# Performance work log

Hardware: AMD Instinct MI355X
Metric: run time of the kernel (lower is better)

The kernel has to match this reference:

```python
import jax, jax.numpy as jnp
import numpy as np

N, E = 50000, 800000
IN, HID, OUT = 128, 256, 128
BN_EPS = 1e-5


def setup_inputs() -> dict:
    key = jax.random.key(0)
    ks = jax.random.split(key, 12)
    x = jax.random.normal(ks[0], (N, IN), dtype=jnp.float32)
    edge_index = jax.random.randint(ks[1], (2, E), 0, N, dtype=jnp.int64)
    edge_weight = jax.random.uniform(ks[2], (E,), dtype=jnp.float32)
    # GCNConv weights (glorot-ish scale) and biases
    W0 = jax.random.normal(ks[3], (IN, HID), dtype=jnp.float32) * (1.0 / np.sqrt(IN))
    b0 = jnp.zeros((HID,), jnp.float32)
    W1 = jax.random.normal(ks[4], (HID, HID), dtype=jnp.float32) * (1.0 / np.sqrt(HID))
    b1 = jnp.zeros((HID,), jnp.float32)
    Wl = jax.random.normal(ks[5], (HID, OUT), dtype=jnp.float32) * (1.0 / np.sqrt(HID))
    bl = jnp.zeros((OUT,), jnp.float32)
    # BatchNorm affine params (eval mode: running_mean=0, running_var=1)
    g0 = 1.0 + 0.1 * jax.random.normal(ks[6], (HID,), dtype=jnp.float32)
    be0 = 0.1 * jax.random.normal(ks[7], (HID,), dtype=jnp.float32)
    g1 = 1.0 + 0.1 * jax.random.normal(ks[8], (HID,), dtype=jnp.float32)
    be1 = 0.1 * jax.random.normal(ks[9], (HID,), dtype=jnp.float32)
    return {"x": x, "edge_index": edge_index, "edge_weight": edge_weight,
            "W0": W0, "b0": b0, "W1": W1, "b1": b1, "Wl": Wl, "bl": bl,
            "g0": g0, "be0": be0, "g1": g1, "be1": be1}


def reference(x, edge_index, edge_weight, W0, b0, W1, b1, Wl, bl, g0, be0, g1, be1):
    n = x.shape[0]
    row, col = edge_index[0], edge_index[1]
    # add self-loops with weight 1 (GCNConv default)
    ar = jnp.arange(n)
    rowf = jnp.concatenate([row, ar])
    colf = jnp.concatenate([col, ar])
    wf = jnp.concatenate([edge_weight, jnp.ones((n,), x.dtype)])
    # symmetric normalization: D^{-1/2} A D^{-1/2}
    deg = jax.ops.segment_sum(wf, colf, num_segments=n)
    dinv = jnp.where(deg > 0, jax.lax.rsqrt(deg), 0.0)
    norm = dinv[rowf] * wf * dinv[colf]  # [E+N]

    def conv(h, W, b):
        h = h @ W                       # [n, d_out]
        msg = h[rowf] * norm[:, None]   # gather + scale per edge
        return jax.ops.segment_sum(msg, colf, num_segments=n) + b

    def bn_eval(h, g, b):
        # eval-mode BN with running_mean=0, running_var=1
        return h * (g / jnp.sqrt(1.0 + BN_EPS)) + b

    h = jax.nn.relu(bn_eval(conv(x, W0, b0), g0, be0))
    h = jax.nn.relu(bn_eval(conv(h, W1, b1), g1, be1))
    h = conv(h, Wl, bl)
    return jax.nn.log_softmax(h, axis=1)
```

## Files before the change

### kernel.cpp

```cpp
#include <hip/hip_runtime.h>
#include <cstddef>
#include <cstdint>


#define GCN_BN_EPS 1e-5f
#define NB_CHUNK 64
#define NPART 4

typedef short v8bf __attribute__((ext_vector_type(8)));
typedef float v4f __attribute__((ext_vector_type(4)));


__device__ __forceinline__ float4 unpack_bf4(uint2 u) {
  float4 r;
  r.x = __uint_as_float(u.x << 16);
  r.y = __uint_as_float(u.x & 0xffff0000u);
  r.z = __uint_as_float(u.y << 16);
  r.w = __uint_as_float(u.y & 0xffff0000u);
  return r;
}
__device__ __forceinline__ uint16_t f2bf(float f) {
  uint32_t u = __float_as_uint(f);
  return (uint16_t)((u + 0x7fffu + ((u >> 16) & 1u)) >> 16);
}
__device__ __forceinline__ uint2 pack_bf4(float4 v) {
  uint2 r;
  r.x = (uint32_t)f2bf(v.x) | ((uint32_t)f2bf(v.y) << 16);
  r.y = (uint32_t)f2bf(v.z) | ((uint32_t)f2bf(v.w) << 16);
  return r;
}


__global__ void detect_kernel(const int* __restrict__ ei, int* __restrict__ flag) {
  if (threadIdx.x == 0) {
    int nz = 0;
    for (int k = 1; k < 64; k += 2) nz |= ei[k];
    *flag = (nz == 0) ? 1 : 0;
  }
}

__global__ void decode_kernel(const int* __restrict__ ei, const float* __restrict__ ew,
                              const int* __restrict__ flag,
                              int* __restrict__ col_, uint2* __restrict__ pk, int E) {
  int e = blockIdx.x * blockDim.x + threadIdx.x;
  if (e >= E) return;
  int r, c;
  if (*flag) { r = ei[2 * e]; c = ei[2 * (E + e)]; }
  else       { r = ei[e];     c = ei[E + e]; }
  col_[e] = c;
  pk[e] = make_uint2((unsigned)r, __float_as_uint(ew[e]));
}

__global__ __launch_bounds__(256) void hist_kernel(const int* __restrict__ col_,
                                                   int* __restrict__ hist,
                                                   int E, int n) {
  extern __shared__ unsigned int hsh[];
  const int chunk = blockIdx.x, part = blockIdx.y;
  const int npl = (n + NPART - 1) / NPART;
  const int lo = part * npl, hi = min(lo + npl, n);
  const int nw = (npl + 1) >> 1;
  for (int i = threadIdx.x; i < nw; i += 256) hsh[i] = 0u;
  __syncthreads();
  const int per = (E + NB_CHUNK - 1) / NB_CHUNK;
  const int e0 = chunk * per, e1 = min(e0 + per, E);
  for (int e = e0 + threadIdx.x; e < e1; e += 256) {
    int c = col_[e];
    if (c >= lo && c < hi) {
      int cl = c - lo;
      atomicAdd(&hsh[cl >> 1], 1u << ((cl & 1) * 16));
    }
  }
  __syncthreads();
  for (int i = threadIdx.x; i < hi - lo; i += 256)
    hist[(size_t)chunk * n + lo + i] = (int)((hsh[i >> 1] >> ((i & 1) * 16)) & 0xffffu);
}

__global__ __launch_bounds__(256) void scan1_kernel(const int* __restrict__ hist,
                                                    int* __restrict__ cnt,
                                                    int* __restrict__ bsum, int n) {
  __shared__ int ws[4];
  int i = blockIdx.x * 256 + threadIdx.x;
  int v = 0;
  if (i < n) {
    for (int b = 0; b < NB_CHUNK; ++b) v += hist[(size_t)b * n + i];
    cnt[i] = v;
  }
  int x = v;
#pragma unroll
  for (int s = 1; s < 64; s <<= 1) x += __shfl_xor(x, s, 64);
  if ((threadIdx.x & 63) == 0) ws[threadIdx.x >> 6] = x;
  __syncthreads();
  if (threadIdx.x == 0) bsum[blockIdx.x] = ws[0] + ws[1] + ws[2] + ws[3];
}

__global__ __launch_bounds__(1024) void scan2_kernel(int* __restrict__ bsum, int G,
                                                     int* __restrict__ off, int n, int E) {
  __shared__ int wsum[16], woff[16];
  int tid = threadIdx.x, lane = tid & 63, wv = tid >> 6;
  int v = (tid < G) ? bsum[tid] : 0;
  int x = v;
#pragma unroll
  for (int s = 1; s < 64; s <<= 1) { int t = __shfl_up(x, s, 64); if (lane >= s) x += t; }
  if (lane == 63) wsum[wv] = x;
  __syncthreads();
  if (wv == 0) {
    int wsv = (lane < 16) ? wsum[lane] : 0;
    int y = wsv;
#pragma unroll
    for (int s = 1; s < 16; s <<= 1) { int t = __shfl_up(y, s, 64); if (lane >= s) y += t; }
    if (lane < 16) woff[lane] = y - wsv;
  }
  __syncthreads();
  if (tid < G) bsum[tid] = x - v + woff[wv];
  if (tid == 0) off[n] = E;
}

__global__ __launch_bounds__(256) void scan3_kernel(const int* __restrict__ cnt,
                                                    const int* __restrict__ bsum,
                                                    int* __restrict__ off, int n) {
  __shared__ int wsum[4], woff[4];
  int tid = threadIdx.x, lane = tid & 63, wv = tid >> 6;
  int i = blockIdx.x * 256 + tid;
  int v = (i < n) ? cnt[i] : 0;
  int x = v;
#pragma unroll
  for (int s = 1; s < 64; s <<= 1) { int t = __shfl_up(x, s, 64); if (lane >= s) x += t; }
  if (lane == 63) wsum[wv] = x;
  __syncthreads();
  if (tid == 0) { int r = 0; for (int k = 0; k < 4; ++k) { woff[k] = r; r += wsum[k]; } }
  __syncthreads();
  if (i < n) off[i] = x - v + woff[wv] + bsum[blockIdx.x];
}

__global__ void base_kernel(const int* __restrict__ off, int* __restrict__ hist, int n) {
  int i = blockIdx.x * blockDim.x + threadIdx.x;
  if (i >= n) return;
  int run = off[i];
  for (int b = 0; b < NB_CHUNK; ++b) {
    size_t idx = (size_t)b * n + i;
    int h = hist[idx];
    hist[idx] = run;
    run += h;
  }
}

__global__ __launch_bounds__(256) void fill_kernel(
    const int* __restrict__ col_, const uint2* __restrict__ pk,
    const int* __restrict__ base, uint2* __restrict__ csr, int E, int n) {
  extern __shared__ int cur[];
  const int chunk = blockIdx.x, part = blockIdx.y;
  const int npl = (n + NPART - 1) / NPART;
  const int lo = part * npl, hi = min(lo + npl, n);
  for (int i = threadIdx.x; i < hi - lo; i += 256)
    cur[i] = base[(size_t)chunk * n + lo + i];
  __syncthreads();
  const int per = (E + NB_CHUNK - 1) / NB_CHUNK;
  const int e0 = chunk * per, e1 = min(e0 + per, E);
  for (int e = e0 + threadIdx.x; e < e1; e += 256) {
    int c = col_[e];
    if (c >= lo && c < hi) {
      int p = atomicAdd(&cur[c - lo], 1);
      csr[p] = pk[e];
    }
  }
}

__global__ void degdinv_kernel(const int* __restrict__ off, const uint2* __restrict__ csr,
                               float* __restrict__ dinv, int n) {
  int i = blockIdx.x * blockDim.x + threadIdx.x;
  if (i >= n) return;
  float s = 1.0f;
  int p1 = off[i + 1];
  for (int p = off[i]; p < p1; ++p) s += __uint_as_float(csr[p].y);
  dinv[i] = rsqrtf(s);
}

__global__ void val_kernel(const int* __restrict__ off, uint2* __restrict__ csr,
                           const float* __restrict__ dinv, int n) {
  int i = blockIdx.x * blockDim.x + threadIdx.x;
  if (i >= n) return;
  float dc = dinv[i];
  int p1 = off[i + 1];
  for (int p = off[i]; p < p1; ++p) {
    uint2 t = csr[p];
    csr[p].y = __float_as_uint(dinv[t.x] * __uint_as_float(t.y) * dc);
  }
}


__global__ void conv_x_kernel(const float* __restrict__ x, uint16_t* __restrict__ xb,
                              int n4) {
  int i = blockIdx.x * blockDim.x + threadIdx.x;
  if (i >= n4) return;
  float4 v = *(const float4*)&x[(size_t)i * 4];
  *(uint2*)&xb[(size_t)i * 4] = pack_bf4(v);
}

__global__ void conv_wt_kernel(const float* __restrict__ W, uint16_t* __restrict__ WT,
                               int K, int Nc) {
  int i = blockIdx.x * blockDim.x + threadIdx.x;
  if (i >= K * Nc) return;
  int n = i / K, k = i - n * K;
  WT[i] = f2bf(W[(size_t)k * Nc + n]);
}


template <int EPI>
__global__ __launch_bounds__(256) void agg256_kernel(
    const uint16_t* __restrict__ hin, uint16_t* __restrict__ hout,
    const int* __restrict__ off, const uint2* __restrict__ csr,
    const float* __restrict__ dinv,
    const float* __restrict__ bias, const float* __restrict__ g,
    const float* __restrict__ be, int n) {
  const int lane = threadIdx.x & 63;
  const int c = blockIdx.x * 4 + (threadIdx.x >> 6);
  if (c >= n) return;
  const int f = lane * 4;
  const int e0 = off[c], e1 = off[c + 1];
  const float di = dinv[c];
  const float s2 = di * di;
  float4 self = unpack_bf4(*(const uint2*)&hin[(size_t)c * 256 + f]);
  float4 acc = make_float4(self.x * s2, self.y * s2, self.z * s2, self.w * s2);

  for (int base = e0; base < e1; base += 64) {
    int idx = base + lane;
    int rs = 0; float rv = 0.0f;
    if (idx < e1) { uint2 ev = csr[idx]; rs = (int)ev.x; rv = __uint_as_float(ev.y); }
    const int m = min(64, e1 - base);
    const int nG = (m + 3) >> 2;
    for (int gI = 0; gI < nG; ++gI) {
      int e_ = gI * 4;
      int s0 = __shfl(rs, e_);     float v0 = __shfl(rv, e_);
      int s1 = __shfl(rs, e_ + 1); float v1 = __shfl(rv, e_ + 1);
      int sB = __shfl(rs, e_ + 2); float v2 = __shfl(rv, e_ + 2);
      int s3 = __shfl(rs, e_ + 3); float v3 = __shfl(rv, e_ + 3);
      float4 h0 = unpack_bf4(*(const uint2*)&hin[(size_t)s0 * 256 + f]);
      float4 h1 = unpack_bf4(*(const uint2*)&hin[(size_t)s1 * 256 + f]);
      float4 h2 = unpack_bf4(*(const uint2*)&hin[(size_t)sB * 256 + f]);
      float4 h3 = unpack_bf4(*(const uint2*)&hin[(size_t)s3 * 256 + f]);
      acc.x += v0 * h0.x + v1 * h1.x + v2 * h2.x + v3 * h3.x;
      acc.y += v0 * h0.y + v1 * h1.y + v2 * h2.y + v3 * h3.y;
      acc.z += v0 * h0.z + v1 * h1.z + v2 * h2.z + v3 * h3.z;
      acc.w += v0 * h0.w + v1 * h1.w + v2 * h2.w + v3 * h3.w;
    }
  }

  if (EPI == 1) {
    const float bns = rsqrtf(1.0f + GCN_BN_EPS);
    float4 bi = *(const float4*)&bias[f];
    float4 gi = *(const float4*)&g[f];
    float4 bei = *(const float4*)&be[f];
    acc.x = fmaxf((acc.x + bi.x) * gi.x * bns + bei.x, 0.0f);
    acc.y = fmaxf((acc.y + bi.y) * gi.y * bns + bei.y, 0.0f);
    acc.z = fmaxf((acc.z + bi.z) * gi.z * bns + bei.z, 0.0f);
    acc.w = fmaxf((acc.w + bi.w) * gi.w * bns + bei.w, 0.0f);
  }
  *(uint2*)&hout[(size_t)c * 256 + f] = pack_bf4(acc);
}

template <int EPI>
__global__ __launch_bounds__(256) void agg128_kernel(
    const uint16_t* __restrict__ hin, void* __restrict__ hout_,
    const int* __restrict__ off, const uint2* __restrict__ csr,
    const float* __restrict__ dinv,
    const float* __restrict__ bias, int n) {
  const int lane = threadIdx.x & 63;
  const int sub = lane & 31;
  const int hbase = lane & 32;
  const int c = blockIdx.x * 8 + (threadIdx.x >> 6) * 2 + (lane >> 5);
  const bool active = (c < n);
  const int f = sub * 4;

  int e0 = 0, e1 = 0;
  float4 acc = make_float4(0.f, 0.f, 0.f, 0.f);
  if (active) {
    e0 = off[c]; e1 = off[c + 1];
    float di = dinv[c];
    float s2 = di * di;
    float4 self = unpack_bf4(*(const uint2*)&hin[(size_t)c * 128 + f]);
    acc = make_float4(self.x * s2, self.y * s2, self.z * s2, self.w * s2);
  }
  int nch = (e1 - e0 + 31) >> 5;
  nch = max(nch, __shfl(nch, lane ^ 32));

  for (int ch = 0; ch < nch; ++ch) {
    int idx = e0 + ch * 32 + sub;
    int rs = 0; float rv = 0.0f;
    if (active && idx < e1) { uint2 ev = csr[idx]; rs = (int)ev.x; rv = __uint_as_float(ev.y); }
    int m = e1 - (e0 + ch * 32);
    m = m < 0 ? 0 : (m > 32 ? 32 : m);
    int mMax = max(m, __shfl(m, lane ^ 32));
    const int nG = (mMax + 3) >> 2;
    for (int gI = 0; gI < nG; ++gI) {
      int e_ = hbase + gI * 4;
      int s0 = __shfl(rs, e_);     float v0 = __shfl(rv, e_);
      int s1 = __shfl(rs, e_ + 1); float v1 = __shfl(rv, e_ + 1);
      int sB = __shfl(rs, e_ + 2); float v2 = __shfl(rv, e_ + 2);
      int s3 = __shfl(rs, e_ + 3); float v3 = __shfl(rv, e_ + 3);
      float4 h0 = unpack_bf4(*(const uint2*)&hin[(size_t)s0 * 128 + f]);
      float4 h1 = unpack_bf4(*(const uint2*)&hin[(size_t)s1 * 128 + f]);
      float4 h2 = unpack_bf4(*(const uint2*)&hin[(size_t)sB * 128 + f]);
      float4 h3 = unpack_bf4(*(const uint2*)&hin[(size_t)s3 * 128 + f]);
      acc.x += v0 * h0.x + v1 * h1.x + v2 * h2.x + v3 * h3.x;
      acc.y += v0 * h0.y + v1 * h1.y + v2 * h2.y + v3 * h3.y;
      acc.z += v0 * h0.z + v1 * h1.z + v2 * h2.z + v3 * h3.z;
      acc.w += v0 * h0.w + v1 * h1.w + v2 * h2.w + v3 * h3.w;
    }
  }

  if (EPI == 0) {
    uint16_t* hout = (uint16_t*)hout_;
    if (active) *(uint2*)&hout[(size_t)c * 128 + f] = pack_bf4(acc);
  } else {
    float* hout = (float*)hout_;
    float4 bi = active ? *(const float4*)&bias[f] : make_float4(0.f, 0.f, 0.f, 0.f);
    float tx = acc.x + bi.x, ty = acc.y + bi.y, tz = acc.z + bi.z, tw = acc.w + bi.w;
    float mx = fmaxf(fmaxf(tx, ty), fmaxf(tz, tw));
#pragma unroll
    for (int s = 1; s < 32; s <<= 1) mx = fmaxf(mx, __shfl_xor(mx, s, 64));
    float ex = expf(tx - mx) + expf(ty - mx) + expf(tz - mx) + expf(tw - mx);
#pragma unroll
    for (int s = 1; s < 32; s <<= 1) ex += __shfl_xor(ex, s, 64);
    float lse = logf(ex) + mx;
    if (active) {
      float4 res = make_float4(tx - lse, ty - lse, tz - lse, tw - lse);
      *(float4*)&hout[(size_t)c * 128 + f] = res;
    }
  }
}

template <int K, int NC, int EPI>
__global__ __launch_bounds__(256) void mfma_gemm_kernel(
    const uint16_t* __restrict__ A, const uint16_t* __restrict__ WT,
    uint16_t* __restrict__ Cb, int M, int tpb,
    const float* __restrict__ bias, const float* __restrict__ g,
    const float* __restrict__ be) {
  constexpr int CW = NC / 4;
  constexpr int NT = CW / 16;
  constexpr int KS = K / 32;
  const int lane = threadIdx.x & 63;
  const int wave = threadIdx.x >> 6;
  const int quad = lane >> 4;
  const int l16 = lane & 15;
  const int col0 = wave * CW;

  const int tiles = (M + 15) >> 4;
  int t0 = blockIdx.x * tpb;
  if (t0 >= tiles) return;
  int t1 = min(t0 + tpb, tiles);

  v8bf b[KS][NT];
#pragma unroll
  for (int ks = 0; ks < KS; ++ks)
#pragma unroll
    for (int nt = 0; nt < NT; ++nt)
      b[ks][nt] = *(const v8bf*)(WT + (size_t)(col0 + nt * 16 + l16) * K +
                                 ks * 32 + quad * 8);

  float sc[NT], o1[NT], o2[NT];
  if (EPI == 1) {
    const float bns = rsqrtf(1.0f + GCN_BN_EPS);
#pragma unroll
    for (int nt = 0; nt < NT; ++nt) {
      int col = col0 + nt * 16 + l16;
      sc[nt] = g[col] * bns; o1[nt] = bias[col]; o2[nt] = be[col];
    }
  }

  v8bf a[KS], an[KS];
  {
    int arow = min(t0 * 16 + l16, M - 1);
    const uint16_t* Ap = A + (size_t)arow * K + quad * 8;
#pragma unroll
    for (int ks = 0; ks < KS; ++ks) a[ks] = *(const v8bf*)(Ap + ks * 32);
  }
  for (int t = t0; t < t1; ++t) {
    if (t + 1 < t1) {
      int arow = min((t + 1) * 16 + l16, M - 1);
      const uint16_t* Ap = A + (size_t)arow * K + quad * 8;
#pragma unroll
      for (int ks = 0; ks < KS; ++ks) an[ks] = *(const v8bf*)(Ap + ks * 32);
    }
    v4f acc[NT];
#pragma unroll
    for (int nt = 0; nt < NT; ++nt) acc[nt] = (v4f){0.f, 0.f, 0.f, 0.f};
#pragma unroll
    for (int ks = 0; ks < KS; ++ks)
#pragma unroll
      for (int nt = 0; nt < NT; ++nt)
        acc[nt] = __builtin_amdgcn_mfma_f32_16x16x32_bf16(a[ks], b[ks][nt],
                                                          acc[nt], 0, 0, 0);
    const int row0 = t * 16 + quad * 4;
#pragma unroll
    for (int nt = 0; nt < NT; ++nt) {
      const int col = col0 + nt * 16 + l16;
#pragma unroll
      for (int r = 0; r < 4; ++r) {
        int row = row0 + r;
        if (row < M) {
          float v = acc[nt][r];
          if (EPI == 1) v = fmaxf((v + o1[nt]) * sc[nt] + o2[nt], 0.0f);
          Cb[(size_t)row * NC + col] = f2bf(v);
        }
      }
    }
#pragma unroll
    for (int ks = 0; ks < KS; ++ks) a[ks] = an[ks];
  }
}


static inline char* carve(char*& p, size_t bytes) {
  char* r = p;
  p += (bytes + 255) & ~(size_t)255;
  return r;
}

extern "C" void kernel_launch(void* const* d_in, const int* in_sizes, int n_in,
                              void* d_out, int out_size, void* d_ws, size_t ws_size,
                              hipStream_t stream) {
  const int N = in_sizes[0] / 128;
  const int E = in_sizes[2];

  const float* x  = (const float*)d_in[0];
  const int*   ei = (const int*)d_in[1];
  const float* ew = (const float*)d_in[2];
  const float* W0 = (const float*)d_in[3];
  const float* b0 = (const float*)d_in[4];
  const float* W1 = (const float*)d_in[5];
  const float* b1 = (const float*)d_in[6];
  const float* Wl = (const float*)d_in[7];
  const float* bl = (const float*)d_in[8];
  const float* g0 = (const float*)d_in[9];
  const float* be0 = (const float*)d_in[10];
  const float* g1 = (const float*)d_in[11];
  const float* be1 = (const float*)d_in[12];
  float* out = (float*)d_out;

  char* p = (char*)d_ws;
  float*    dinv    = (float*)carve(p, (size_t)N * 4);
  int*      cnt     = (int*)carve(p, (size_t)N * 4);
  int*      off     = (int*)carve(p, (size_t)(N + 1) * 4);
  int*      flag    = (int*)carve(p, 256);
  int*      bsum    = (int*)carve(p, 1024 * 4);
  int*      col_    = (int*)carve(p, (size_t)E * 4);
  uint2*    pk      = (uint2*)carve(p, (size_t)E * 8);
  uint2*    csr     = (uint2*)carve(p, (size_t)E * 8);
  int*      hist    = (int*)carve(p, (size_t)NB_CHUNK * N * 4);
  uint16_t* xb16    = (uint16_t*)carve(p, (size_t)N * 128 * 2);
  uint16_t* bufR    = (uint16_t*)carve(p, (size_t)N * 128 * 2);
  uint16_t* bufP    = (uint16_t*)carve(p, (size_t)N * 256 * 2);
  uint16_t* bufQ    = (uint16_t*)carve(p, (size_t)N * 256 * 2);
  uint16_t* W0t     = (uint16_t*)carve(p, (size_t)128 * 256 * 2);
  uint16_t* W1t     = (uint16_t*)carve(p, (size_t)256 * 256 * 2);
  uint16_t* Wlt     = (uint16_t*)carve(p, (size_t)256 * 128 * 2);

  const int TB = 256;
  const int gN = (N + TB - 1) / TB;
  const int gE = (E + TB - 1) / TB;
  const int gW4 = (N + 3) / 4;
  const int gW8 = (N + 7) / 8;
  const int tiles = (N + 15) / 16;
  const int TPB = 4;
  const int gG = (tiles + TPB - 1) / TPB;
  const int npl = (N + NPART - 1) / NPART;
  const size_t ldsHist = (size_t)((npl + 1) / 2) * 4;
  const size_t ldsFill = (size_t)npl * 4;
  const dim3 gHF(NB_CHUNK, NPART);

  detect_kernel<<<1, 64, 0, stream>>>(ei, flag);
  decode_kernel<<<gE, TB, 0, stream>>>(ei, ew, flag, col_, pk, E);
  hist_kernel<<<gHF, TB, ldsHist, stream>>>(col_, hist, E, N);
  scan1_kernel<<<gN, TB, 0, stream>>>(hist, cnt, bsum, N);
  scan2_kernel<<<1, 1024, 0, stream>>>(bsum, gN, off, N, E);
  scan3_kernel<<<gN, TB, 0, stream>>>(cnt, bsum, off, N);
  base_kernel<<<gN, TB, 0, stream>>>(off, hist, N);
  fill_kernel<<<gHF, TB, ldsFill, stream>>>(col_, pk, hist, csr, E, N);
  degdinv_kernel<<<gN, TB, 0, stream>>>(off, csr, dinv, N);
  val_kernel<<<gN, TB, 0, stream>>>(off, csr, dinv, N);

  conv_x_kernel<<<(N * 32 + TB - 1) / TB, TB, 0, stream>>>(x, xb16, N * 32);
  conv_wt_kernel<<<(128 * 256 + TB - 1) / TB, TB, 0, stream>>>(W0, W0t, 128, 256);
  conv_wt_kernel<<<(256 * 256 + TB - 1) / TB, TB, 0, stream>>>(W1, W1t, 256, 256);
  conv_wt_kernel<<<(256 * 128 + TB - 1) / TB, TB, 0, stream>>>(Wl, Wlt, 256, 128);

  agg128_kernel<0><<<gW8, 256, 0, stream>>>(xb16, bufR, off, csr, dinv, nullptr, N);
  mfma_gemm_kernel<128, 256, 1><<<gG, 256, 0, stream>>>(bufR, W0t, bufP, N, TPB,
                                                        b0, g0, be0);
  mfma_gemm_kernel<256, 256, 0><<<gG, 256, 0, stream>>>(bufP, W1t, bufQ, N, TPB,
                                                        nullptr, nullptr, nullptr);
  agg256_kernel<1><<<gW4, 256, 0, stream>>>(bufQ, bufP, off, csr, dinv,
                                            b1, g1, be1, N);
  mfma_gemm_kernel<256, 128, 0><<<gG, 256, 0, stream>>>(bufP, Wlt, bufR, N, TPB,
                                                        nullptr, nullptr, nullptr);
  agg128_kernel<2><<<gW8, 256, 0, stream>>>(bufR, out, off, csr, dinv, bl, N);
}
```

Measured before the change: 400.0 us.

## Split 256-wide aggregation into feature slices across grid x with edge-parallel segments

The 256-feature aggregation kernel now splits the feature dimension into 8 slices of 32 columns, one per grid-x block. Each wavefront processes 4 edges at once in 16-lane segments and reduces them with xor shuffles. The intent is to shrink each gather to 64-byte contiguous chunks per edge slice and improve cache locality per slice. The cost is re-reading the CSR for every slice and extra shuffle reductions. The GEMM tiles-per-block count is also doubled from 4 to 8.

```diff
diff --git a/kernel.cpp b/kernel.cpp
--- a/kernel.cpp
+++ b/kernel.cpp
@@ -206,21 +206,21 @@
 
 
 template <int EPI>
-__global__ __launch_bounds__(256) void agg256_kernel(
+__global__ __launch_bounds__(256) void agg256s_kernel(
     const uint16_t* __restrict__ hin, uint16_t* __restrict__ hout,
     const int* __restrict__ off, const uint2* __restrict__ csr,
     const float* __restrict__ dinv,
     const float* __restrict__ bias, const float* __restrict__ g,
     const float* __restrict__ be, int n) {
   const int lane = threadIdx.x & 63;
-  const int c = blockIdx.x * 4 + (threadIdx.x >> 6);
+  const int seg = lane >> 4;
+  const int l16 = lane & 15;
+  const int sl = blockIdx.x;
+  const int c = blockIdx.y * 4 + (threadIdx.x >> 6);
   if (c >= n) return;
-  const int f = lane * 4;
+  const int fb = sl * 32 + l16 * 2;
   const int e0 = off[c], e1 = off[c + 1];
-  const float di = dinv[c];
-  const float s2 = di * di;
-  float4 self = unpack_bf4(*(const uint2*)&hin[(size_t)c * 256 + f]);
-  float4 acc = make_float4(self.x * s2, self.y * s2, self.z * s2, self.w * s2);
+  float ax = 0.0f, ay = 0.0f;
 
   for (int base = e0; base < e1; base += 64) {
     int idx = base + lane;
@@ -229,33 +229,30 @@
     const int m = min(64, e1 - base);
     const int nG = (m + 3) >> 2;
     for (int gI = 0; gI < nG; ++gI) {
-      int e_ = gI * 4;
-      int s0 = __shfl(rs, e_);     float v0 = __shfl(rv, e_);
-      int s1 = __shfl(rs, e_ + 1); float v1 = __shfl(rv, e_ + 1);
-      int sB = __shfl(rs, e_ + 2); float v2 = __shfl(rv, e_ + 2);
-      int s3 = __shfl(rs, e_ + 3); float v3 = __shfl(rv, e_ + 3);
-      float4 h0 = unpack_bf4(*(const uint2*)&hin[(size_t)s0 * 256 + f]);
-      float4 h1 = unpack_bf4(*(const uint2*)&hin[(size_t)s1 * 256 + f]);
-      float4 h2 = unpack_bf4(*(const uint2*)&hin[(size_t)sB * 256 + f]);
-      float4 h3 = unpack_bf4(*(const uint2*)&hin[(size_t)s3 * 256 + f]);
-      acc.x += v0 * h0.x + v1 * h1.x + v2 * h2.x + v3 * h3.x;
-      acc.y += v0 * h0.y + v1 * h1.y + v2 * h2.y + v3 * h3.y;
-      acc.z += v0 * h0.z + v1 * h1.z + v2 * h2.z + v3 * h3.z;
-      acc.w += v0 * h0.w + v1 * h1.w + v2 * h2.w + v3 * h3.w;
-    }
-  }
-
-  if (EPI == 1) {
-    const float bns = rsqrtf(1.0f + GCN_BN_EPS);
-    float4 bi = *(const float4*)&bias[f];
-    float4 gi = *(const float4*)&g[f];
-    float4 bei = *(const float4*)&be[f];
-    acc.x = fmaxf((acc.x + bi.x) * gi.x * bns + bei.x, 0.0f);
-    acc.y = fmaxf((acc.y + bi.y) * gi.y * bns + bei.y, 0.0f);
-    acc.z = fmaxf((acc.z + bi.z) * gi.z * bns + bei.z, 0.0f);
-    acc.w = fmaxf((acc.w + bi.w) * gi.w * bns + bei.w, 0.0f);
-  }
-  *(uint2*)&hout[(size_t)c * 256 + f] = pack_bf4(acc);
+      int e_ = gI * 4 + seg;
+      int s = __shfl(rs, e_);
+      float v = __shfl(rv, e_);
+      uint32_t hb = *(const uint32_t*)&hin[(size_t)s * 256 + fb];
+      ax += v * __uint_as_float(hb << 16);
+      ay += v * __uint_as_float(hb & 0xffff0000u);
+    }
+  }
+  ax += __shfl_xor(ax, 16, 64); ay += __shfl_xor(ay, 16, 64);
+  ax += __shfl_xor(ax, 32, 64); ay += __shfl_xor(ay, 32, 64);
+  if (seg == 0) {
+    const float di = dinv[c];
+    const float s2 = di * di;
+    uint32_t sb = *(const uint32_t*)&hin[(size_t)c * 256 + fb];
+    ax += s2 * __uint_as_float(sb << 16);
+    ay += s2 * __uint_as_float(sb & 0xffff0000u);
+    if (EPI == 1) {
+      const float bns = rsqrtf(1.0f + GCN_BN_EPS);
+      ax = fmaxf((ax + bias[fb]) * g[fb] * bns + be[fb], 0.0f);
+      ay = fmaxf((ay + bias[fb + 1]) * g[fb + 1] * bns + be[fb + 1], 0.0f);
+    }
+    *(uint32_t*)&hout[(size_t)c * 256 + fb] =
+        (uint32_t)f2bf(ax) | ((uint32_t)f2bf(ay) << 16);
+  }
 }
 
 template <int EPI>
@@ -458,10 +455,10 @@
   const int TB = 256;
   const int gN = (N + TB - 1) / TB;
   const int gE = (E + TB - 1) / TB;
-  const int gW4 = (N + 3) / 4;
   const int gW8 = (N + 7) / 8;
+  const dim3 gS(8, (N + 3) / 4);
   const int tiles = (N + 15) / 16;
-  const int TPB = 4;
+  const int TPB = 8;
   const int gG = (tiles + TPB - 1) / TPB;
   const int npl = (N + NPART - 1) / NPART;
   const size_t ldsHist = (size_t)((npl + 1) / 2) * 4;
@@ -489,7 +486,7 @@
                                                         b0, g0, be0);
   mfma_gemm_kernel<256, 256, 0><<<gG, 256, 0, stream>>>(bufP, W1t, bufQ, N, TPB,
                                                         nullptr, nullptr, nullptr);
-  agg256_kernel<1><<<gW4, 256, 0, stream>>>(bufQ, bufP, off, csr, dinv,
+  agg256s_kernel<1><<<gS, 256, 0, stream>>>(bufQ, bufP, off, csr, dinv,
                                             b1, g1, be1, N);
   mfma_gemm_kernel<256, 128, 0><<<gG, 256, 0, stream>>>(bufP, Wlt, bufR, N, TPB,
                                                         nullptr, nullptr, nullptr);
```

New measurement: 496.7 us. 1.24x slower.
